# Kernel tuning notes

Hardware: AMD Instinct MI355X
Metric: run time of the kernel (lower is better)

Reference implementation:

```python
import jax, jax.numpy as jnp
import numpy as np

EPS = 1e-05
IFAVERAGE = True


def setup_inputs() -> dict:
    key = jax.random.key(0)
    k1, k2 = jax.random.split(key)
    B, C = 4, 5
    D = H = W = 128
    inp = jax.random.normal(k1, (B, C, D, H, W), dtype=jnp.float32)
    tgt = jax.random.randint(k2, (B, D, H, W), 0, C, dtype=jnp.int64)
    return {"input": inp, "target": tgt}


def reference(input, target):
    B, C = input.shape[0], input.shape[1]
    x = input.reshape(B, C, -1)          # (B, C, N)
    t = target.reshape(B, -1)            # (B, N)
    pred = jnp.argmax(x, axis=1)         # (B, N) int, matches torch.max(dim=-2) indices

    def per_batch_counts(p, tg):
        pred_c = jnp.bincount(p, length=C)                              # (C,)
        tgt_c = jnp.bincount(tg, length=C)                              # (C,)
        # intersection: count positions where pred == target, binned by class
        inter_c = jnp.bincount(jnp.where(p == tg, p, C), length=C + 1)[:C]
        return pred_c, tgt_c, inter_c

    pred_c, tgt_c, inter_c = jax.vmap(per_batch_counts)(pred, t)        # each (B, C)

    # classes 1..C-1 (background class 0 excluded)
    inter = inter_c[:, 1:].astype(jnp.float32)
    union = (pred_c[:, 1:] + tgt_c[:, 1:]).astype(jnp.float32)
    dice = (2.0 * inter + EPS) / (union + EPS)                          # (B, C-1)

    if IFAVERAGE:
        out = jnp.mean(jnp.mean(dice, axis=0), axis=0, keepdims=True)   # shape (1,)
    else:
        out = dice
    return out
```

## Files before the change

### kernel.cpp

```cpp
#include <hip/hip_runtime.h>


static constexpr int   kB   = 4;
static constexpr int   kC   = 5;
static constexpr int   kN   = 128 * 128 * 128;
static constexpr float kEPS = 1e-5f;

static constexpr int TPB   = 256;
static constexpr int ITERS = 4;
static constexpr int GPB   = TPB * ITERS;
static constexpr int BPB   = (kN / 4) / GPB;
static constexpr int NBLK  = kB * BPB;

__device__ __forceinline__ int argmax5(float v0, float v1, float v2, float v3, float v4) {
    int bi = 0; float bv = v0;
    if (v1 > bv) { bv = v1; bi = 1; }
    if (v2 > bv) { bv = v2; bi = 2; }
    if (v3 > bv) { bv = v3; bi = 3; }
    if (v4 > bv) { bv = v4; bi = 4; }
    return bi;
}

__device__ __forceinline__ void acc1(int p, int t,
                                     unsigned& P, unsigned& T, unsigned& I) {
    unsigned pm = p ? (1u << ((p - 1) << 3)) : 0u;
    unsigned tm = t ? (1u << ((t - 1) << 3)) : 0u;
    P += pm;
    T += tm;
    I += (p == t) ? pm : 0u;
}

__global__ __launch_bounds__(TPB) void dice_count_kernel(
        const float* __restrict__ in, const int* __restrict__ tgt,
        unsigned* __restrict__ partial)
{
    const int bg  = blockIdx.x;
    const int b   = bg >> 9;
    const int blk = bg & 511;
    const float* inb = in  + (size_t)b * kC * kN;
    const int*   tb  = tgt + (size_t)b * kN;

    const float4* c0 = (const float4*)(inb + 0 * (size_t)kN);
    const float4* c1 = (const float4*)(inb + 1 * (size_t)kN);
    const float4* c2 = (const float4*)(inb + 2 * (size_t)kN);
    const float4* c3 = (const float4*)(inb + 3 * (size_t)kN);
    const float4* c4 = (const float4*)(inb + 4 * (size_t)kN);
    const int4*   tp = (const int4*)tb;

    const int base = blk * GPB + threadIdx.x;

    unsigned P = 0, T = 0, I = 0;
#pragma unroll 2
    for (int i = 0; i < ITERS; ++i) {
        const int n4 = base + i * TPB;
        float4 v0 = c0[n4];
        float4 v1 = c1[n4];
        float4 v2 = c2[n4];
        float4 v3 = c3[n4];
        float4 v4 = c4[n4];
        int4   t4 = tp[n4];
        acc1(argmax5(v0.x, v1.x, v2.x, v3.x, v4.x), t4.x, P, T, I);
        acc1(argmax5(v0.y, v1.y, v2.y, v3.y, v4.y), t4.y, P, T, I);
        acc1(argmax5(v0.z, v1.z, v2.z, v3.z, v4.z), t4.z, P, T, I);
        acc1(argmax5(v0.w, v1.w, v2.w, v3.w, v4.w), t4.w, P, T, I);
    }

    unsigned r[6];
    r[0] = P & 0x00FF00FFu;  r[1] = (P >> 8) & 0x00FF00FFu;
    r[2] = T & 0x00FF00FFu;  r[3] = (T >> 8) & 0x00FF00FFu;
    r[4] = I & 0x00FF00FFu;  r[5] = (I >> 8) & 0x00FF00FFu;

#pragma unroll
    for (int k = 0; k < 6; ++k) {
#pragma unroll
        for (int off = 32; off > 0; off >>= 1) {
            r[k] += (unsigned)__shfl_down((int)r[k], off, 64);
        }
    }

    __shared__ unsigned sred[4][6];
    const int wave = threadIdx.x >> 6;
    if ((threadIdx.x & 63) == 0) {
#pragma unroll
        for (int k = 0; k < 6; ++k) sred[wave][k] = r[k];
    }
    __syncthreads();

    if (threadIdx.x < 6) {
        const int j = threadIdx.x;
        unsigned s = sred[0][j] + sred[1][j] + sred[2][j] + sred[3][j];
        const int g   = j >> 1;
        const int kLo = j & 1;
        unsigned* dst = partial + bg * 12 + g * 4;
        dst[kLo]     = s & 0xFFFFu;
        dst[kLo + 2] = s >> 16;
    }
}

__global__ __launch_bounds__(256) void dice_reduce_kernel(
        const unsigned* __restrict__ partial, float* __restrict__ out)
{
    unsigned acc[4][12];
#pragma unroll
    for (int b = 0; b < 4; ++b)
#pragma unroll
        for (int j = 0; j < 12; ++j) acc[b][j] = 0;

#pragma unroll
    for (int c = 0; c < 8; ++c) {
        const int b  = c >> 1;
        const int bg = c * 256 + threadIdx.x;
        const uint4* p = (const uint4*)(partial + bg * 12);
        uint4 x = p[0], y = p[1], z = p[2];
        acc[b][0] += x.x; acc[b][1]  += x.y; acc[b][2]  += x.z; acc[b][3]  += x.w;
        acc[b][4] += y.x; acc[b][5]  += y.y; acc[b][6]  += y.z; acc[b][7]  += y.w;
        acc[b][8] += z.x; acc[b][9]  += z.y; acc[b][10] += z.z; acc[b][11] += z.w;
    }

#pragma unroll
    for (int b = 0; b < 4; ++b)
#pragma unroll
        for (int j = 0; j < 12; ++j)
#pragma unroll
            for (int off = 32; off > 0; off >>= 1)
                acc[b][j] += (unsigned)__shfl_down((int)acc[b][j], off, 64);

    __shared__ unsigned part[4][48];
    const int wave = threadIdx.x >> 6;
    if ((threadIdx.x & 63) == 0) {
#pragma unroll
        for (int b = 0; b < 4; ++b)
#pragma unroll
            for (int j = 0; j < 12; ++j) part[wave][b * 12 + j] = acc[b][j];
    }
    __syncthreads();

    __shared__ unsigned tot[48];
    if (threadIdx.x < 48) {
        const int t = threadIdx.x;
        tot[t] = part[0][t] + part[1][t] + part[2][t] + part[3][t];
    }
    __syncthreads();

    if (threadIdx.x < 16) {
        const int b = threadIdx.x >> 2;
        const int k = threadIdx.x & 3;
        float pr = (float)tot[b * 12 + 0 + k];
        float tg = (float)tot[b * 12 + 4 + k];
        float it = (float)tot[b * 12 + 8 + k];
        float d = (2.0f * it + kEPS) / (pr + tg + kEPS);
#pragma unroll
        for (int off = 8; off > 0; off >>= 1) d += __shfl_down(d, off, 16);
        if (threadIdx.x == 0) out[0] = d * (1.0f / 16.0f);
    }
}

extern "C" void kernel_launch(void* const* d_in, const int* in_sizes, int n_in,
                              void* d_out, int out_size, void* d_ws, size_t ws_size,
                              hipStream_t stream) {
    const float* in  = (const float*)d_in[0];
    const int*   tgt = (const int*)d_in[1];
    float*       out = (float*)d_out;
    unsigned*    partial = (unsigned*)d_ws;

    dice_count_kernel<<<dim3(NBLK), dim3(TPB), 0, stream>>>(in, tgt, partial);
    dice_reduce_kernel<<<dim3(1), dim3(256), 0, stream>>>(partial, out);
}
```

Measured before the change: 254.9 us.

## Stage inputs through LDS with async global_load_lds and halve per-block work

Replaces direct vectorized global loads with asynchronous global-to-LDS transfers (global_load_lds, 16 bytes per lane) of all five channels plus the target into a 48 KB shared buffer, then computes argmax and counts from LDS. Each block now handles 512 float4 groups instead of 1024, doubling the block count, and the reduce kernel reads 16 partials per thread to match. The goal is more memory requests in flight without holding registers for them. The cost is a large LDS footprint per block, which limits occupancy, plus a barrier and extra partial sums.

```diff
diff --git a/kernel.cpp b/kernel.cpp
--- a/kernel.cpp
+++ b/kernel.cpp
@@ -6,11 +6,10 @@
 static constexpr int   kN   = 128 * 128 * 128;
 static constexpr float kEPS = 1e-5f;
 
-static constexpr int TPB   = 256;
-static constexpr int ITERS = 4;
-static constexpr int GPB   = TPB * ITERS;
-static constexpr int BPB   = (kN / 4) / GPB;
-static constexpr int NBLK  = kB * BPB;
+static constexpr int TPB  = 256;
+static constexpr int GPC  = 512;
+static constexpr int BPB  = (kN / 4) / GPC;
+static constexpr int NBLK = kB * BPB;
 
 __device__ __forceinline__ int argmax5(float v0, float v1, float v2, float v3, float v4) {
     int bi = 0; float bv = v0;
@@ -30,35 +29,51 @@
     I += (p == t) ? pm : 0u;
 }
 
+#define GLOBAL_TO_LDS(gp, lp)                                                   \
+    __builtin_amdgcn_global_load_lds(                                           \
+        (const __attribute__((address_space(1))) void*)(gp),                    \
+        (__attribute__((address_space(3))) void*)(lp), 16, 0, 0)
+
 __global__ __launch_bounds__(TPB) void dice_count_kernel(
         const float* __restrict__ in, const int* __restrict__ tgt,
         unsigned* __restrict__ partial)
 {
+    __shared__ float4 lds4[6 * GPC];
+
     const int bg  = blockIdx.x;
-    const int b   = bg >> 9;
-    const int blk = bg & 511;
+    const int b   = bg >> 10;
+    const int blk = bg & 1023;
     const float* inb = in  + (size_t)b * kC * kN;
     const int*   tb  = tgt + (size_t)b * kN;
 
-    const float4* c0 = (const float4*)(inb + 0 * (size_t)kN);
-    const float4* c1 = (const float4*)(inb + 1 * (size_t)kN);
-    const float4* c2 = (const float4*)(inb + 2 * (size_t)kN);
-    const float4* c3 = (const float4*)(inb + 3 * (size_t)kN);
-    const float4* c4 = (const float4*)(inb + 4 * (size_t)kN);
-    const int4*   tp = (const int4*)tb;
+    const size_t chunk0 = (size_t)blk * GPC;
+    const int wv = threadIdx.x >> 6;
+    const int ln = threadIdx.x & 63;
 
-    const int base = blk * GPB + threadIdx.x;
+#pragma unroll
+    for (int p = 0; p < 2; ++p) {
+        const int    gb = p * 256 + wv * 64;
+        const size_t g0 = chunk0 + gb + ln;
+#pragma unroll
+        for (int s = 0; s < 5; ++s) {
+            const float4* gp = (const float4*)(inb + (size_t)s * kN) + g0;
+            GLOBAL_TO_LDS(gp, &lds4[s * GPC + gb + ln]);
+        }
+        const int4* gt = (const int4*)tb + g0;
+        GLOBAL_TO_LDS(gt, &lds4[5 * GPC + gb + ln]);
+    }
+    __syncthreads();
 
     unsigned P = 0, T = 0, I = 0;
-#pragma unroll 2
-    for (int i = 0; i < ITERS; ++i) {
-        const int n4 = base + i * TPB;
-        float4 v0 = c0[n4];
-        float4 v1 = c1[n4];
-        float4 v2 = c2[n4];
-        float4 v3 = c3[n4];
-        float4 v4 = c4[n4];
-        int4   t4 = tp[n4];
+#pragma unroll
+    for (int p = 0; p < 2; ++p) {
+        const int g = p * 256 + threadIdx.x;
+        float4 v0 = lds4[0 * GPC + g];
+        float4 v1 = lds4[1 * GPC + g];
+        float4 v2 = lds4[2 * GPC + g];
+        float4 v3 = lds4[3 * GPC + g];
+        float4 v4 = lds4[4 * GPC + g];
+        int4   t4 = ((const int4*)lds4)[5 * GPC + g];
         acc1(argmax5(v0.x, v1.x, v2.x, v3.x, v4.x), t4.x, P, T, I);
         acc1(argmax5(v0.y, v1.y, v2.y, v3.y, v4.y), t4.y, P, T, I);
         acc1(argmax5(v0.z, v1.z, v2.z, v3.z, v4.z), t4.z, P, T, I);
@@ -79,10 +94,9 @@
     }
 
     __shared__ unsigned sred[4][6];
-    const int wave = threadIdx.x >> 6;
-    if ((threadIdx.x & 63) == 0) {
+    if (ln == 0) {
 #pragma unroll
-        for (int k = 0; k < 6; ++k) sred[wave][k] = r[k];
+        for (int k = 0; k < 6; ++k) sred[wv][k] = r[k];
     }
     __syncthreads();
 
@@ -107,8 +121,8 @@
         for (int j = 0; j < 12; ++j) acc[b][j] = 0;
 
 #pragma unroll
-    for (int c = 0; c < 8; ++c) {
-        const int b  = c >> 1;
+    for (int c = 0; c < 16; ++c) {
+        const int b  = c >> 2;
         const int bg = c * 256 + threadIdx.x;
         const uint4* p = (const uint4*)(partial + bg * 12);
         uint4 x = p[0], y = p[1], z = p[2];
```

Result: no change. 257.5 us (+1.1%).
